# Optimization experiments

Hardware: AMD Instinct MI355X
Metric: run time of the kernel (lower is better)

The kernel has to match this reference:

```python
import jax, jax.numpy as jnp
import numpy as np

N_NODES = 75000
N_EDGES = 1200000
IN_FEATS = 64
OUT_FEATS = 64


def setup_inputs() -> dict:
    key = jax.random.key(0)
    k1, k2, k3, k4, k5 = jax.random.split(key, 5)
    feature = jax.random.normal(k1, (N_NODES, IN_FEATS), dtype=jnp.float32)
    src = jax.random.randint(k2, (N_EDGES,), 0, N_NODES, dtype=jnp.int32)
    dst = jax.random.randint(k3, (N_EDGES,), 0, N_NODES, dtype=jnp.int32)
    # degree: in-degree + 1 (clamped >= 1 so sqrt/div are well-defined), float32 node data
    deg = np.bincount(np.asarray(dst), minlength=N_NODES).astype(np.float32) + 1.0
    degree = jnp.asarray(deg)
    W = jax.random.normal(k4, (IN_FEATS, OUT_FEATS), dtype=jnp.float32) * (1.0 / np.sqrt(IN_FEATS))
    b = jax.random.normal(k5, (OUT_FEATS,), dtype=jnp.float32) * 0.01
    return {"feature": feature, "degree": degree, "src": src, "dst": dst, "W": W, "b": b}


def reference(feature, degree, src, dst, W, b):
    # message: m_e = h[src_e] / sqrt(degree[src_e])   -> [E, F]
    inv_sqrt_deg = 1.0 / jnp.sqrt(degree)
    m = feature[src] * inv_sqrt_deg[src][:, None]
    # reduce: sum messages into destination nodes      -> [N, F]
    agg = jax.ops.segment_sum(m, dst, num_segments=feature.shape[0])
    # node apply: h = (agg / sqrt(degree)) @ W + b     -> [N, O]
    h = agg * inv_sqrt_deg[:, None]
    return h @ W + b
```

## Files before the change

### kernel.cpp

```cpp
#include <hip/hip_runtime.h>

#define FEATS 64
#define PSZ   64
#define MAXP  1280
#define PSCH  4688
#define SPT   512
#define PEPT  10
#define NCH   256
#define CAPP  2560

typedef __attribute__((ext_vector_type(8))) short short8;
typedef __attribute__((ext_vector_type(4))) float floatx4;

static __device__ __forceinline__ unsigned short f2bf(float f) {
    const unsigned int u = __float_as_uint(f);
    return (unsigned short)((u + 0x7FFFu + ((u >> 16) & 1u)) >> 16);
}
static __device__ __forceinline__ float bflo(unsigned int u) {
    return __uint_as_float(u << 16);
}
static __device__ __forceinline__ float bfhi(unsigned int u) {
    return __uint_as_float(u & 0xFFFF0000u);
}

__global__ __launch_bounds__(256) void convert_k(
        const float* __restrict__ degree,
        const float* __restrict__ feature,
        const float* __restrict__ Wm,
        unsigned short* __restrict__ Fs16,
        unsigned short* __restrict__ WtB,
        int n_nodes) {
    const int gtid = blockIdx.x * 256 + threadIdx.x;
    const int total = n_nodes * 8;
    const float4* f4 = (const float4*)feature;
    uint4* o4 = (uint4*)Fs16;
    for (int ch = gtid; ch < total; ch += 2048 * 256) {
        const float w = rsqrtf(degree[ch >> 3]);
        const float4 fa = f4[ch * 2];
        const float4 fb = f4[ch * 2 + 1];
        uint4 o;
        o.x = (unsigned int)f2bf(fa.x * w) | ((unsigned int)f2bf(fa.y * w) << 16);
        o.y = (unsigned int)f2bf(fa.z * w) | ((unsigned int)f2bf(fa.w * w) << 16);
        o.z = (unsigned int)f2bf(fb.x * w) | ((unsigned int)f2bf(fb.y * w) << 16);
        o.w = (unsigned int)f2bf(fb.z * w) | ((unsigned int)f2bf(fb.w * w) << 16);
        o4[ch] = o;
    }
    if (blockIdx.x == 0) {
        if (threadIdx.x < FEATS) Fs16[(size_t)n_nodes * FEATS + threadIdx.x] = 0;
        for (int idx = threadIdx.x; idx < FEATS * FEATS; idx += 256) {
            const int k = idx >> 6, n = idx & 63;
            WtB[n * FEATS + k] = f2bf(Wm[idx]);
        }
    }
}

__global__ __launch_bounds__(SPT) void prep_sort(
        const int* __restrict__ src,
        const int* __restrict__ dst,
        int* __restrict__ slab,
        unsigned short* __restrict__ runoffT,
        int n_edges, int np, int nbs) {
    __shared__ int cnt[MAXP];
    __shared__ int swt[8];
    __shared__ __align__(16) int sval[PSCH];
    const int tid = threadIdx.x;
    const int lane = tid & 63;
    const int wv = tid >> 6;
    const int b = blockIdx.x;

    for (int i = tid; i < np; i += SPT) cnt[i] = 0;
    __syncthreads();

    const int estart = b * PSCH;
    const int eend = min(estart + PSCH, n_edges);
    const int mb = eend - estart;

    int dv[PEPT];
#pragma unroll
    for (int k = 0; k < PEPT; ++k) {
        const int e = estart + tid + k * SPT;
        dv[k] = (e < eend) ? dst[e] : -1;
    }
    int prk[PEPT];
#pragma unroll
    for (int k = 0; k < PEPT; ++k) {
        prk[k] = 0;
        if (dv[k] >= 0) {
            const int d = dv[k];
            const int p = d >> 6;
            const int r = atomicAdd(&cnt[p], 1);
            prk[k] = p | (r << 11) | ((d & 63) << 24);
        }
    }
    __syncthreads();

    int my[3];
    int psum = 0;
    const int p0 = tid * 3;
#pragma unroll
    for (int j = 0; j < 3; ++j) {
        const int p = p0 + j;
        my[j] = psum;
        if (p < np) psum += cnt[p];
    }
    int x = psum;
#pragma unroll
    for (int off = 1; off < 64; off <<= 1) {
        const int v = __shfl_up(x, off);
        if (lane >= off) x += v;
    }
    if (lane == 63) swt[wv] = x;
    __syncthreads();
    int wbase = 0;
#pragma unroll
    for (int w = 0; w < 8; ++w) if (w < wv) wbase += swt[w];
    const int tbase = wbase + (x - psum);
#pragma unroll
    for (int j = 0; j < 3; ++j) {
        const int p = p0 + j;
        if (p < np) cnt[p] = tbase + my[j];
    }
    __syncthreads();

#pragma unroll
    for (int k = 0; k < PEPT; ++k) {
        const int e = estart + tid + k * SPT;
        if (e < eend) {
            const int pr = prk[k];
            const int p = pr & 2047;
            const int r = (pr >> 11) & 8191;
            const int dl = (pr >> 24) & 63;
            sval[cnt[p] + r] = (src[e] & 0x1FFFF) | (dl << 17);
        }
    }
    __syncthreads();

    int* so = slab + estart;
    const int m4 = mb >> 2;
    int4* so4 = (int4*)so;
    const int4* sv4 = (const int4*)sval;
    for (int i = tid; i < m4; i += SPT) so4[i] = sv4[i];
    for (int i = (m4 << 2) + tid; i < mb; i += SPT) so[i] = sval[i];
    for (int i = tid; i <= np; i += SPT)
        runoffT[(size_t)i * nbs + b] = (unsigned short)((i < np) ? cnt[i] : mb);
}

__global__ __launch_bounds__(512, 8) void gather_apply11(
        const int* __restrict__ slab,
        const unsigned short* __restrict__ runoffT,
        const float* __restrict__ degree,
        const unsigned short* __restrict__ Fs16,
        const unsigned short* __restrict__ WtB,
        const float* __restrict__ bias,
        float* __restrict__ out,
        int n_nodes, int np, int nbs) {
    __shared__ __align__(16) int ledges[CAPP];
    __shared__ __align__(16) unsigned short saggb[PSZ * 72];
    __shared__ int boffA[PSZ + 1];
    __shared__ int bcur[PSZ];
    __shared__ float swinv[PSZ];

    const int tid = threadIdx.x;
    const int lane = tid & 63;
    const int wv = tid >> 6;

    int p;
    {
        const int bid = blockIdx.x;
        const int q = np >> 3, r = np & 7;
        const int xcd = bid & 7, idx = bid >> 3;
        p = ((xcd < r) ? xcd * (q + 1) : r * (q + 1) + (xcd - r) * q) + idx;
    }
    const int n0 = p * PSZ;
    const int nn = min(PSZ, n_nodes - n0);

    if (tid < PSZ) bcur[tid] = 0;
    if (wv == 0) {
        const float dg = (lane < nn) ? degree[n0 + lane] : 1.0f;
        swinv[lane] = rsqrtf(dg);
        const int c = (lane < nn) ? ((int)(dg + 0.5f) - 1) : 0;
        const int cp = (c + 7) & ~7;
        int x = cp;
#pragma unroll
        for (int off = 1; off < 64; off <<= 1) {
            const int v = __shfl_up(x, off);
            if (lane >= off) x += v;
        }
        if (lane == 0) boffA[0] = 0;
        boffA[lane + 1] = x;
    }
    __syncthreads();
    const int mpad = boffA[PSZ];

    if (mpad <= CAPP) {
        for (int i = tid; i < mpad; i += SPT) ledges[i] = n_nodes;
        __syncthreads();
        for (int t = tid; t < nbs * 4; t += SPT) {
            const int rr = t >> 2, sub = t & 3;
            const int st = runoffT[(size_t)p * nbs + rr];
            const int en = runoffT[(size_t)(p + 1) * nbs + rr];
            const int* g = slab + (size_t)rr * PSCH;
            for (int q = st + sub; q < en; q += 4) {
                const int rec = g[q];
                const int dl = (rec >> 17) & 63;
                const int pos = boffA[dl] + atomicAdd(&bcur[dl], 1);
                if (pos < mpad) ledges[pos] = rec & 0x1FFFF;
            }
        }
        __syncthreads();

        const int q4 = lane >> 4;
        const int c16 = lane & 15;
        const uint2* FsU2 = (const uint2*)Fs16;
        for (int n = wv; n < PSZ; n += 8) {
            const int st = boffA[n];
            const int en8 = boffA[n + 1];
            float a0 = 0.f, a1 = 0.f, a2 = 0.f, a3 = 0.f;
            float c0 = 0.f, c1 = 0.f, c2 = 0.f, c3 = 0.f;
#pragma unroll 2
            for (int j = st; j < en8; j += 8) {
                const int r0 = ledges[j + q4];
                const int r1 = ledges[j + 4 + q4];
                const uint2 u0 = FsU2[((size_t)r0 << 4) + c16];
                const uint2 u1 = FsU2[((size_t)r1 << 4) + c16];
                a0 += bflo(u0.x); a1 += bfhi(u0.x);
                a2 += bflo(u0.y); a3 += bfhi(u0.y);
                c0 += bflo(u1.x); c1 += bfhi(u1.x);
                c2 += bflo(u1.y); c3 += bfhi(u1.y);
            }
            float v0 = a0 + c0, v1 = a1 + c1, v2 = a2 + c2, v3 = a3 + c3;
            v0 += __shfl(v0, lane ^ 16); v0 += __shfl(v0, lane ^ 32);
            v1 += __shfl(v1, lane ^ 16); v1 += __shfl(v1, lane ^ 32);
            v2 += __shfl(v2, lane ^ 16); v2 += __shfl(v2, lane ^ 32);
            v3 += __shfl(v3, lane ^ 16); v3 += __shfl(v3, lane ^ 32);
            if (q4 == 0) {
                const unsigned int pk0 =
                    (unsigned int)f2bf(v0) | ((unsigned int)f2bf(v1) << 16);
                const unsigned int pk1 =
                    (unsigned int)f2bf(v2) | ((unsigned int)f2bf(v3) << 16);
                uint2* dp = (uint2*)(saggb + n * 72 + c16 * 4);
                *dp = make_uint2(pk0, pk1);
            }
        }
    } else {
        __syncthreads();
        __syncthreads();
        for (int n = wv; n < PSZ; n += 8) {
            float acc = 0.f;
            for (int c = 0; c < nbs; ++c) {
                const int st = runoffT[(size_t)p * nbs + c];
                const int en = runoffT[(size_t)(p + 1) * nbs + c];
                const int* g = slab + (size_t)c * PSCH;
                for (int i = st; i < en; ++i) {
                    const int rec = g[i];
                    if (((rec >> 17) & 63) == n) {
                        const unsigned int us =
                            Fs16[((size_t)(rec & 0x1FFFF) << 6) + lane];
                        acc += __uint_as_float(us << 16);
                    }
                }
            }
            saggb[n * 72 + lane] = f2bf(acc);
        }
    }
    __syncthreads();

    const int col = lane & 15;
    const int quad = lane >> 4;
    const int mt = wv >> 1;
    const int nh = (wv & 1) << 1;
    floatx4 acc[2] = {};
#pragma unroll
    for (int kt = 0; kt < 2; ++kt) {
        const short8 af = *(const short8*)(saggb + (mt * 16 + col) * 72 + kt * 32 + quad * 8);
#pragma unroll
        for (int t = 0; t < 2; ++t) {
            const int nt = nh + t;
            const short8 bf = *(const short8*)((const short*)WtB + (nt * 16 + col) * FEATS + kt * 32 + quad * 8);
            acc[t] = __builtin_amdgcn_mfma_f32_16x16x32_bf16(af, bf, acc[t], 0, 0, 0);
        }
    }
#pragma unroll
    for (int t = 0; t < 2; ++t) {
        const int nt = nh + t;
        const float bv = bias[nt * 16 + col];
#pragma unroll
        for (int r = 0; r < 4; ++r) {
            const int row = mt * 16 + quad * 4 + r;
            if (row < nn)
                out[(size_t)(n0 + row) * FEATS + nt * 16 + col] = swinv[row] * acc[t][r] + bv;
        }
    }
}

static inline size_t align256(size_t x) { return (x + 255) & ~(size_t)255; }

extern "C" void kernel_launch(void* const* d_in, const int* in_sizes, int n_in,
                              void* d_out, int out_size, void* d_ws, size_t ws_size,
                              hipStream_t stream) {
    const float* feature = (const float*)d_in[0];
    const float* degree  = (const float*)d_in[1];
    const int*   src     = (const int*)d_in[2];
    const int*   dst     = (const int*)d_in[3];
    const float* Wm      = (const float*)d_in[4];
    const float* bias    = (const float*)d_in[5];
    float* out = (float*)d_out;

    const int n_nodes = in_sizes[1];
    const int n_edges = in_sizes[2];
    const int np = (n_nodes + PSZ - 1) / PSZ;
    const int nbs = NCH;

    char* ws = (char*)d_ws;
    unsigned short* Fs16 = (unsigned short*)ws; ws += align256(((size_t)n_nodes + 1) * FEATS * 2);
    unsigned short* WtB  = (unsigned short*)ws; ws += align256((size_t)FEATS * FEATS * 2);
    int* slab = (int*)ws;                       ws += align256((size_t)NCH * PSCH * 4);
    unsigned short* runoffT = (unsigned short*)ws; ws += align256((size_t)(np + 1) * NCH * 2);

    convert_k<<<2048, 256, 0, stream>>>(degree, feature, Wm, Fs16, WtB, n_nodes);
    prep_sort<<<nbs, SPT, 0, stream>>>(src, dst, slab, runoffT, n_edges, np, nbs);
    gather_apply11<<<np, SPT, 0, stream>>>(slab, runoffT, degree, Fs16, WtB, bias, out,
                                           n_nodes, np, nbs);
}
```

Baseline: 130.2 us.

## Fuse feature conversion into sort kernel and prefetch src early

The bf16 feature conversion and W transpose now run as extra blocks of the edge-sort kernel instead of a separate launch, so one kernel boundary goes away and the two independent jobs can overlap on the GPU. The src indices are loaded into registers before the scan barrier rather than after it, hiding their latency. The gather loop unroll goes from 2 to 4. The trade-offs are a heavier shared-memory footprint for the conversion blocks, which inherit the sort kernel's LDS allocation and may lower occupancy, and more registers in the gather loop.

```diff
diff --git a/kernel.cpp b/kernel.cpp
--- a/kernel.cpp
+++ b/kernel.cpp
@@ -23,43 +23,17 @@
     return __uint_as_float(u & 0xFFFF0000u);
 }
 
-__global__ __launch_bounds__(256) void convert_k(
+__global__ __launch_bounds__(SPT) void prep_fused(
         const float* __restrict__ degree,
         const float* __restrict__ feature,
         const float* __restrict__ Wm,
+        const int* __restrict__ src,
+        const int* __restrict__ dst,
         unsigned short* __restrict__ Fs16,
         unsigned short* __restrict__ WtB,
-        int n_nodes) {
-    const int gtid = blockIdx.x * 256 + threadIdx.x;
-    const int total = n_nodes * 8;
-    const float4* f4 = (const float4*)feature;
-    uint4* o4 = (uint4*)Fs16;
-    for (int ch = gtid; ch < total; ch += 2048 * 256) {
-        const float w = rsqrtf(degree[ch >> 3]);
-        const float4 fa = f4[ch * 2];
-        const float4 fb = f4[ch * 2 + 1];
-        uint4 o;
-        o.x = (unsigned int)f2bf(fa.x * w) | ((unsigned int)f2bf(fa.y * w) << 16);
-        o.y = (unsigned int)f2bf(fa.z * w) | ((unsigned int)f2bf(fa.w * w) << 16);
-        o.z = (unsigned int)f2bf(fb.x * w) | ((unsigned int)f2bf(fb.y * w) << 16);
-        o.w = (unsigned int)f2bf(fb.z * w) | ((unsigned int)f2bf(fb.w * w) << 16);
-        o4[ch] = o;
-    }
-    if (blockIdx.x == 0) {
-        if (threadIdx.x < FEATS) Fs16[(size_t)n_nodes * FEATS + threadIdx.x] = 0;
-        for (int idx = threadIdx.x; idx < FEATS * FEATS; idx += 256) {
-            const int k = idx >> 6, n = idx & 63;
-            WtB[n * FEATS + k] = f2bf(Wm[idx]);
-        }
-    }
-}
-
-__global__ __launch_bounds__(SPT) void prep_sort(
-        const int* __restrict__ src,
-        const int* __restrict__ dst,
         int* __restrict__ slab,
         unsigned short* __restrict__ runoffT,
-        int n_edges, int np, int nbs) {
+        int n_nodes, int n_edges, int np, int nbs) {
     __shared__ int cnt[MAXP];
     __shared__ int swt[8];
     __shared__ __align__(16) int sval[PSCH];
@@ -68,6 +42,31 @@
     const int wv = tid >> 6;
     const int b = blockIdx.x;
 
+    if (b >= nbs) {
+        const int idx = (b - nbs) * SPT + tid;
+        const int total = n_nodes * 8;
+        if (idx < total) {
+            const float w = rsqrtf(degree[idx >> 3]);
+            const float4* f4 = (const float4*)feature;
+            const float4 fa = f4[idx * 2];
+            const float4 fb = f4[idx * 2 + 1];
+            uint4 o;
+            o.x = (unsigned int)f2bf(fa.x * w) | ((unsigned int)f2bf(fa.y * w) << 16);
+            o.y = (unsigned int)f2bf(fa.z * w) | ((unsigned int)f2bf(fa.w * w) << 16);
+            o.z = (unsigned int)f2bf(fb.x * w) | ((unsigned int)f2bf(fb.y * w) << 16);
+            o.w = (unsigned int)f2bf(fb.z * w) | ((unsigned int)f2bf(fb.w * w) << 16);
+            ((uint4*)Fs16)[idx] = o;
+        }
+        if (b == nbs) {
+            if (tid < FEATS) Fs16[(size_t)n_nodes * FEATS + tid] = 0;
+            for (int i = tid; i < FEATS * FEATS; i += SPT) {
+                const int k = i >> 6, n = i & 63;
+                WtB[n * FEATS + k] = f2bf(Wm[i]);
+            }
+        }
+        return;
+    }
+
     for (int i = tid; i < np; i += SPT) cnt[i] = 0;
     __syncthreads();
 
@@ -92,6 +91,12 @@
             prk[k] = p | (r << 11) | ((d & 63) << 24);
         }
     }
+    int sv[PEPT];
+#pragma unroll
+    for (int k = 0; k < PEPT; ++k) {
+        const int e = estart + tid + k * SPT;
+        sv[k] = (e < eend) ? src[e] : 0;
+    }
     __syncthreads();
 
     int my[3];
@@ -124,13 +129,12 @@
 
 #pragma unroll
     for (int k = 0; k < PEPT; ++k) {
-        const int e = estart + tid + k * SPT;
-        if (e < eend) {
+        if (dv[k] >= 0) {
             const int pr = prk[k];
             const int p = pr & 2047;
             const int r = (pr >> 11) & 8191;
             const int dl = (pr >> 24) & 63;
-            sval[cnt[p] + r] = (src[e] & 0x1FFFF) | (dl << 17);
+            sval[cnt[p] + r] = (sv[k] & 0x1FFFF) | (dl << 17);
         }
     }
     __syncthreads();
@@ -145,7 +149,7 @@
         runoffT[(size_t)i * nbs + b] = (unsigned short)((i < np) ? cnt[i] : mb);
 }
 
-__global__ __launch_bounds__(512, 8) void gather_apply11(
+__global__ __launch_bounds__(512, 8) void gather_apply12(
         const int* __restrict__ slab,
         const unsigned short* __restrict__ runoffT,
         const float* __restrict__ degree,
@@ -217,7 +221,7 @@
             const int en8 = boffA[n + 1];
             float a0 = 0.f, a1 = 0.f, a2 = 0.f, a3 = 0.f;
             float c0 = 0.f, c1 = 0.f, c2 = 0.f, c3 = 0.f;
-#pragma unroll 2
+#pragma unroll 4
             for (int j = st; j < en8; j += 8) {
                 const int r0 = ledges[j + q4];
                 const int r1 = ledges[j + 4 + q4];
@@ -310,6 +314,7 @@
     const int n_edges = in_sizes[2];
     const int np = (n_nodes + PSZ - 1) / PSZ;
     const int nbs = NCH;
+    const int ncv = (n_nodes * 8 + SPT - 1) / SPT;
 
     char* ws = (char*)d_ws;
     unsigned short* Fs16 = (unsigned short*)ws; ws += align256(((size_t)n_nodes + 1) * FEATS * 2);
@@ -317,8 +322,9 @@
     int* slab = (int*)ws;                       ws += align256((size_t)NCH * PSCH * 4);
     unsigned short* runoffT = (unsigned short*)ws; ws += align256((size_t)(np + 1) * NCH * 2);
 
-    convert_k<<<2048, 256, 0, stream>>>(degree, feature, Wm, Fs16, WtB, n_nodes);
-    prep_sort<<<nbs, SPT, 0, stream>>>(src, dst, slab, runoffT, n_edges, np, nbs);
-    gather_apply11<<<np, SPT, 0, stream>>>(slab, runoffT, degree, Fs16, WtB, bias, out,
+    prep_fused<<<nbs + ncv, SPT, 0, stream>>>(degree, feature, Wm, src, dst,
+                                              Fs16, WtB, slab, runoffT,
+                                              n_nodes, n_edges, np, nbs);
+    gather_apply12<<<np, SPT, 0, stream>>>(slab, runoffT, degree, Fs16, WtB, bias, out,
                                            n_nodes, np, nbs);
 }
```

Result: no change. 128.9 us (-1.0%).
